# Optimization experiments

Hardware: AMD Instinct MI355X
Metric: run time of the kernel (lower is better)

The kernel has to match this reference:

```python
import jax, jax.numpy as jnp
import numpy as np

N, C_IN, F = 64, 1024, 20          # batch, backbone channels, grid size (640/32)
N_CLASSES = 80
A = 3                               # anchors in this layer (mask [6,7,8])
STRIDE = 32
C = N_CLASSES + 5                   # 85
C_OUT = A * C                       # 255
ANCHORS = np.array([[116.0, 90.0], [156.0, 198.0], [373.0, 326.0]], np.float32) / STRIDE


def setup_inputs() -> dict:
    key = jax.random.key(0)
    k1, k2 = jax.random.split(key)
    xin = jax.random.normal(k1, (N, C_IN, F, F), jnp.float32)
    conv_w = jax.random.normal(k2, (C_OUT, C_IN, 1, 1), jnp.float32) * 0.02
    conv_b = jnp.zeros((C_OUT,), jnp.float32)
    return {"xin": xin, "conv_w": conv_w, "conv_b": conv_b}


def reference(xin, conv_w, conv_b):
    anchors = jnp.asarray(ANCHORS, dtype=xin.dtype)  # [A, 2], grid units
    # 1x1 conv head: [N, C_OUT, F, F]
    out = jax.lax.conv_general_dilated(xin, conv_w, window_strides=(1, 1),
                                       padding="VALID")
    out = out + conv_b[None, :, None, None]
    # [N, A, C, F, F] -> [N, A, F(y), F(x), C]
    out = out.reshape(N, A, C, F, F).transpose(0, 1, 3, 4, 2)

    xy = jax.nn.sigmoid(out[..., :2])       # sigmoid on tx, ty
    wh = out[..., 2:4]                      # raw tw, th
    objcls = jax.nn.sigmoid(out[..., 4:])   # sigmoid on obj + classes

    grid = jnp.arange(F, dtype=xin.dtype)
    px = xy[..., 0] + grid[None, None, None, :]   # + x_shift (varies along last spatial dim)
    py = xy[..., 1] + grid[None, None, :, None]   # + y_shift
    pw = jnp.exp(wh[..., 0]) * anchors[:, 0].reshape(1, A, 1, 1)
    ph = jnp.exp(wh[..., 1]) * anchors[:, 1].reshape(1, A, 1, 1)

    boxes = jnp.stack([px, py, pw, ph], axis=-1) * STRIDE  # back to pixel coords
    pred = jnp.concatenate([boxes, objcls], axis=-1)       # [N, A, F, F, C]
    return pred.reshape(N, -1, C)                           # [N, A*F*F, C]
```

## Files before the change

### kernel.cpp

```cpp
#include <hip/hip_runtime.h>
#include <hip/hip_bf16.h>
#include <math.h>

#define CIN    1024
#define S_TOT  400
#define COUT   255
#define NCH    85
#define NIMG   64
#define NFLAT  (NIMG * S_TOT)
#define BN     128
#define BK     64
#define NSTEP  16
#define NTHR   512

#define BB        32768
#define LDS_BYTES 49152
#define WSTEP_B   32768

typedef __attribute__((ext_vector_type(8))) short bf16x8;
typedef __attribute__((ext_vector_type(4))) float f32x4;

struct __attribute__((aligned(4))) f4u { float x, y, z, w; };

__device__ __forceinline__ int wOff(int co, int kg) {
    return (co << 7) + ((kg << 4) ^ ((co & 7) << 4));
}
__device__ __forceinline__ int xBoff(int s, int kg) {
    return BB + (s << 7) + ((kg << 4) ^ (((s >> 1) & 7) << 4));
}

__device__ __forceinline__ unsigned pk2(float a, float b) {
    __hip_bfloat162 h;
    h.x = __float2bfloat16(a);
    h.y = __float2bfloat16(b);
    return *reinterpret_cast<unsigned*>(&h);
}

__device__ __forceinline__ float sigmoidf_(float v) {
    return 1.0f / (1.0f + expf(-v));
}

__device__ __forceinline__ void gload_lds16(const void* g, void* l) {
    __builtin_amdgcn_global_load_lds(
        (const __attribute__((address_space(1))) unsigned int*)g,
        (__attribute__((address_space(3))) unsigned int*)l,
        16, 0, 0);
}

__global__ __launch_bounds__(256) void w_pre(const float* __restrict__ w,
                                             unsigned short* __restrict__ wbf) {
    int g = blockIdx.x * 256 + threadIdx.x;
    int co    = g >> 7;
    int kgAll = g & 127;
    int k     = kgAll << 3;
    int step  = k >> 6;
    int kg    = (k >> 3) & 7;
    union { unsigned short u[8]; bf16x8 v; } pk;
    if (co < COUT) {
        const float* src = w + (size_t)co * CIN + k;
        #pragma unroll
        for (int j = 0; j < 8; ++j) {
            __hip_bfloat16 h = __float2bfloat16(src[j]);
            pk.u[j] = *reinterpret_cast<unsigned short*>(&h);
        }
    } else {
        #pragma unroll
        for (int j = 0; j < 8; ++j) pk.u[j] = 0;
    }
    char* dst = reinterpret_cast<char*>(wbf) + step * WSTEP_B + wOff(co, kg);
    *reinterpret_cast<bf16x8*>(dst) = pk.v;
}

__global__ __launch_bounds__(NTHR, 2) void yolo_m97(
    const float* __restrict__ xin,
    const unsigned short* __restrict__ wbf,
    const float* __restrict__ bias,
    float* __restrict__ out)
{
    __shared__ __align__(16) char smem[LDS_BYTES];

    const int tile = blockIdx.x * BN;
    const int tid  = threadIdx.x;
    const int lane = tid & 63;
    const int w8   = tid >> 6;
    const int llo  = lane & 15;
    const int lhi  = lane >> 4;
    const int co_w = (w8 >> 1) * 64;
    const int s_w  = (w8 & 1) * 64;

    const int bllo = tid & 31;
    const int bgrp = tid >> 5;
    const int flatB = tile + 4 * bllo;
    const int nB = flatB / S_TOT;
    const int sB = flatB - nB * S_TOT;
    const float* xsrcB = xin + ((size_t)nB * CIN + bgrp * 8) * S_TOT + sB;

    f32x4 acc[4][4] = {};

    for (int t = 0; t < NSTEP; ++t) {
        const char* wg = (const char*)wbf + (size_t)t * WSTEP_B;
        #pragma unroll
        for (int i = 0; i < 4; ++i)
            gload_lds16(wg + i * 8192 + (size_t)tid * 16,
                        smem + i * 8192 + w8 * 1024);

        if (tid < 256) {
            const float* src = xsrcB + (size_t)t * (BK * S_TOT);
            union F4 { float4 v; float f[4]; } cu[8];
            #pragma unroll
            for (int j = 0; j < 8; ++j) cu[j].v = *(const float4*)(src + j * S_TOT);
            #pragma unroll
            for (int r = 0; r < 4; ++r) {
                union { unsigned u4[4]; bf16x8 b; } rr;
                #pragma unroll
                for (int jj = 0; jj < 4; ++jj)
                    rr.u4[jj] = pk2(cu[2 * jj].f[r], cu[2 * jj + 1].f[r]);
                *(bf16x8*)(smem + xBoff(4 * bllo + r, bgrp)) = rr.b;
            }
        }
        __syncthreads();

        #pragma unroll
        for (int ks = 0; ks < 2; ++ks) {
            const int kgr = ks * 4 + lhi;
            bf16x8 afr[4], bfr[4];
            #pragma unroll
            for (int mi = 0; mi < 4; ++mi)
                afr[mi] = *(bf16x8*)(smem + wOff(co_w + mi * 16 + llo, kgr));
            #pragma unroll
            for (int ns = 0; ns < 4; ++ns)
                bfr[ns] = *(bf16x8*)(smem + xBoff(s_w + ns * 16 + llo, kgr));
            #pragma unroll
            for (int mi = 0; mi < 4; ++mi)
                #pragma unroll
                for (int ns = 0; ns < 4; ++ns)
                    acc[mi][ns] = __builtin_amdgcn_mfma_f32_16x16x32_bf16(
                        afr[mi], bfr[ns], acc[mi][ns], 0, 0, 0);
        }
        __syncthreads();
    }

    const float anchW[3] = {116.0f, 156.0f, 373.0f};
    const float anchH[3] = {90.0f, 198.0f, 326.0f};

    #pragma unroll
    for (int mi = 0; mi < 4; ++mi) {
        const int co0 = co_w + mi * 16 + lhi * 4;
        const int aW  = co0 / NCH;
        const int c0  = co0 - aW * NCH;
        const bool whole = (c0 <= NCH - 4) && (co0 + 3 < COUT);
        float bv[4];
        #pragma unroll
        for (int r = 0; r < 4; ++r)
            bv[r] = (co0 + r < COUT) ? bias[co0 + r] : 0.0f;

        #pragma unroll
        for (int ns = 0; ns < 4; ++ns) {
            const int flat = tile + s_w + ns * 16 + llo;
            const int n = flat / S_TOT;
            const int s = flat - n * S_TOT;
            const float sx = (float)(s % 20);
            const float sy = (float)(s / 20);
            if (whole) {
                float r4[4];
                #pragma unroll
                for (int r = 0; r < 4; ++r) {
                    const int c = c0 + r;
                    const float v = acc[mi][ns][r] + bv[r];
                    float res;
                    if (c == 0)      res = (sigmoidf_(v) + sx) * 32.0f;
                    else if (c == 1) res = (sigmoidf_(v) + sy) * 32.0f;
                    else if (c == 2) res = expf(v) * anchW[aW];
                    else if (c == 3) res = expf(v) * anchH[aW];
                    else             res = sigmoidf_(v);
                    r4[r] = res;
                }
                f4u* pp = (f4u*)(out + (size_t)n * 102000 + aW * 34000 + s * 85 + c0);
                f4u val = {r4[0], r4[1], r4[2], r4[3]};
                *pp = val;
            } else {
                #pragma unroll
                for (int r = 0; r < 4; ++r) {
                    const int co = co0 + r;
                    if (co < COUT) {
                        const int a2 = co / NCH;
                        const int c  = co - a2 * NCH;
                        const float v = acc[mi][ns][r] + bv[r];
                        float res;
                        if (c == 0)      res = (sigmoidf_(v) + sx) * 32.0f;
                        else if (c == 1) res = (sigmoidf_(v) + sy) * 32.0f;
                        else if (c == 2) res = expf(v) * anchW[a2];
                        else if (c == 3) res = expf(v) * anchH[a2];
                        else             res = sigmoidf_(v);
                        out[(size_t)n * 102000 + a2 * 34000 + s * 85 + c] = res;
                    }
                }
            }
        }
    }
}

extern "C" void kernel_launch(void* const* d_in, const int* in_sizes, int n_in,
                              void* d_out, int out_size, void* d_ws, size_t ws_size,
                              hipStream_t stream) {
    const float* xin  = (const float*)d_in[0];
    const float* w    = (const float*)d_in[1];
    const float* bias = (const float*)d_in[2];
    float* out = (float*)d_out;
    unsigned short* wbf = (unsigned short*)d_ws;

    w_pre<<<128, 256, 0, stream>>>(w, wbf);
    yolo_m97<<<NFLAT / BN, NTHR, 0, stream>>>(xin, wbf, bias, out);
}
```

Baseline: 72.92 us.

## Stage epilogue output through LDS for contiguous coalesced global stores

The epilogue now writes activated results into shared memory in the output layout, 32 spatial positions at a time, and then has all threads copy contiguous 16-byte chunks to global memory. Before, each lane stored scattered float4 values with a stride of 85 floats, which coalesced poorly. The cost is four extra rounds of LDS write, barrier and read, plus index arithmetic per chunk. Only half the waves do the activation work in each round, so that part is serialized.

```diff
diff --git a/kernel.cpp b/kernel.cpp
--- a/kernel.cpp
+++ b/kernel.cpp
@@ -71,7 +71,7 @@
     *reinterpret_cast<bf16x8*>(dst) = pk.v;
 }
 
-__global__ __launch_bounds__(NTHR, 2) void yolo_m97(
+__global__ __launch_bounds__(NTHR, 2) void yolo_dw(
     const float* __restrict__ xin,
     const unsigned short* __restrict__ wbf,
     const float* __restrict__ bias,
@@ -142,61 +142,77 @@
 
     const float anchW[3] = {116.0f, 156.0f, 373.0f};
     const float anchH[3] = {90.0f, 198.0f, 326.0f};
-
-    #pragma unroll
-    for (int mi = 0; mi < 4; ++mi) {
-        const int co0 = co_w + mi * 16 + lhi * 4;
-        const int aW  = co0 / NCH;
-        const int c0  = co0 - aW * NCH;
-        const bool whole = (c0 <= NCH - 4) && (co0 + 3 < COUT);
-        float bv[4];
-        #pragma unroll
-        for (int r = 0; r < 4; ++r)
-            bv[r] = (co0 + r < COUT) ? bias[co0 + r] : 0.0f;
-
-        #pragma unroll
-        for (int ns = 0; ns < 4; ++ns) {
-            const int flat = tile + s_w + ns * 16 + llo;
-            const int n = flat / S_TOT;
-            const int s = flat - n * S_TOT;
-            const float sx = (float)(s % 20);
-            const float sy = (float)(s / 20);
-            if (whole) {
-                float r4[4];
+    float* lout = (float*)smem;
+
+    for (int ch = 0; ch < 4; ++ch) {
+        if ((w8 & 1) == (ch >> 1)) {
+            const int nsb = (ch & 1) * 2;
+            #pragma unroll
+            for (int nsi = 0; nsi < 2; ++nsi) {
+                const int ns = nsb + nsi;
+                const int flat = tile + s_w + ns * 16 + llo;
+                const int s = flat % S_TOT;
+                const float sx = (float)(s % 20);
+                const float sy = (float)(s / 20);
+                const int sl = nsi * 16 + llo;
                 #pragma unroll
-                for (int r = 0; r < 4; ++r) {
-                    const int c = c0 + r;
-                    const float v = acc[mi][ns][r] + bv[r];
-                    float res;
-                    if (c == 0)      res = (sigmoidf_(v) + sx) * 32.0f;
-                    else if (c == 1) res = (sigmoidf_(v) + sy) * 32.0f;
-                    else if (c == 2) res = expf(v) * anchW[aW];
-                    else if (c == 3) res = expf(v) * anchH[aW];
-                    else             res = sigmoidf_(v);
-                    r4[r] = res;
-                }
-                f4u* pp = (f4u*)(out + (size_t)n * 102000 + aW * 34000 + s * 85 + c0);
-                f4u val = {r4[0], r4[1], r4[2], r4[3]};
-                *pp = val;
-            } else {
-                #pragma unroll
-                for (int r = 0; r < 4; ++r) {
-                    const int co = co0 + r;
-                    if (co < COUT) {
-                        const int a2 = co / NCH;
-                        const int c  = co - a2 * NCH;
-                        const float v = acc[mi][ns][r] + bv[r];
-                        float res;
-                        if (c == 0)      res = (sigmoidf_(v) + sx) * 32.0f;
-                        else if (c == 1) res = (sigmoidf_(v) + sy) * 32.0f;
-                        else if (c == 2) res = expf(v) * anchW[a2];
-                        else if (c == 3) res = expf(v) * anchH[a2];
-                        else             res = sigmoidf_(v);
-                        out[(size_t)n * 102000 + a2 * 34000 + s * 85 + c] = res;
+                for (int mi = 0; mi < 4; ++mi) {
+                    #pragma unroll
+                    for (int r = 0; r < 4; ++r) {
+                        const int co = co_w + mi * 16 + lhi * 4 + r;
+                        if (co < COUT) {
+                            const int a = co / NCH;
+                            const int c = co - a * NCH;
+                            const float v = acc[mi][ns][r] + bias[co];
+                            float res;
+                            if (c == 0)      res = (sigmoidf_(v) + sx) * 32.0f;
+                            else if (c == 1) res = (sigmoidf_(v) + sy) * 32.0f;
+                            else if (c == 2) res = expf(v) * anchW[a];
+                            else if (c == 3) res = expf(v) * anchH[a];
+                            else             res = sigmoidf_(v);
+                            lout[a * 2720 + sl * 85 + c] = res;
+                        }
                     }
                 }
             }
         }
+        __syncthreads();
+
+        #pragma unroll
+        for (int p = 0; p < 4; ++p) {
+            const int idx = p * NTHR + tid;
+            if (idx < 2040) {
+                const int b    = idx << 4;
+                const int a    = b / 10880;
+                const int boff = b - a * 10880;
+                const int sl0  = boff / 340;
+                const int c0   = (boff - sl0 * 340) >> 2;
+                const int fl0  = tile + ch * 32 + sl0;
+                const int n0   = fl0 / S_TOT;
+                const int s0   = fl0 - n0 * S_TOT;
+                const int sl3  = (boff + 12) / 340;
+                const int fl3  = tile + ch * 32 + sl3;
+                f32x4 v = *(const f32x4*)(smem + a * 10880 + boff);
+                if (fl3 / S_TOT == n0) {
+                    f4u* dst = (f4u*)(out + (size_t)n0 * 102000 + a * 34000
+                                      + s0 * 85 + c0);
+                    f4u val = {v[0], v[1], v[2], v[3]};
+                    *dst = val;
+                } else {
+                    #pragma unroll
+                    for (int e = 0; e < 4; ++e) {
+                        const int bf  = boff + 4 * e;
+                        const int sle = bf / 340;
+                        const int fle = tile + ch * 32 + sle;
+                        const int ne  = fle / S_TOT;
+                        const int se  = fle - ne * S_TOT;
+                        const int ce  = (bf - sle * 340) >> 2;
+                        out[(size_t)ne * 102000 + a * 34000 + se * 85 + ce] = v[e];
+                    }
+                }
+            }
+        }
+        __syncthreads();
     }
 }
 
@@ -210,5 +226,5 @@
     unsigned short* wbf = (unsigned short*)d_ws;
 
     w_pre<<<128, 256, 0, stream>>>(w, wbf);
-    yolo_m97<<<NFLAT / BN, NTHR, 0, stream>>>(xin, wbf, bias, out);
-}
+    yolo_dw<<<NFLAT / BN, NTHR, 0, stream>>>(xin, wbf, bias, out);
+}
```

Measured after the change: 255.2 us. 250% more time.
